# Performance work log

Measured on AMD Instinct MI355X. Metric: run time of the kernel, lower is better.

The kernel has to match this reference:

```python
import jax, jax.numpy as jnp
import numpy as np

B, S, F_IN, F_OUT = 8, 128, 768, 768
NUM_REL = 41           # num_dependencies + 1
NUM_LAYER = 2
N_HEAD, HID = 8, 96    # hidden_dim = embed_dim // n_head
EMB = 768


def setup_inputs() -> dict:
    key = jax.random.key(0)
    ks = jax.random.split(key, 14)
    s = 1.0 / np.sqrt(F_IN)
    inp = {
        "x": jax.random.normal(ks[0], (B, S, F_IN), dtype=jnp.float32),
        "adj": jax.random.uniform(ks[1], (B, NUM_REL, S, S), dtype=jnp.float32),
        "q": jax.random.normal(ks[2], (B, EMB), dtype=jnp.float32),
        # R-GCN params (stacked over layers)
        "w_rgcn": jax.random.uniform(ks[3], (NUM_LAYER, NUM_REL, F_IN, F_OUT), minval=-s, maxval=s),
        "score_w": jax.random.uniform(ks[4], (NUM_LAYER, F_OUT), minval=-s, maxval=s),
        "score_b": jax.random.uniform(ks[5], (NUM_LAYER,), minval=-s, maxval=s),
        # Attention params (stored as [in, out] for x @ W)
        "wk": jax.random.uniform(ks[6], (EMB, N_HEAD * HID), minval=-s, maxval=s),
        "bk": jnp.zeros((N_HEAD * HID,), jnp.float32),
        "wq": jax.random.uniform(ks[7], (EMB, N_HEAD * HID), minval=-s, maxval=s),
        "bq": jnp.zeros((N_HEAD * HID,), jnp.float32),
        "wbil": jax.random.uniform(ks[8], (HID, HID), minval=-1.0 / np.sqrt(HID), maxval=1.0 / np.sqrt(HID)),
        "wproj": jax.random.uniform(ks[9], (N_HEAD * HID, EMB), minval=-s, maxval=s),
        "bproj": jnp.zeros((EMB,), jnp.float32),
    }
    return inp


def _rgcn_layer(h, adj, w, sw, sb):
    # h: [B,S,I]; adj: [B,R,S,S]; w: [R,I,O]
    hidden = jnp.einsum("bsi,rio->brso", h, w)            # per-relation transform
    denom = jnp.sum(adj, axis=3, keepdims=True)           # [B,R,S,1]
    intm = jnp.einsum("brsk,brko->brso", adj, hidden)     # relation-wise aggregation
    div = intm / jnp.where(denom == 0, jnp.ones_like(denom), denom)
    logits = jnp.einsum("brso,o->brs", div, sw) + sb      # score Linear(out->1)
    r_coeffs = jax.nn.softmax(logits, axis=1)             # softmax over relations
    out = jnp.einsum("brso,brs->bso", div, r_coeffs)
    return jax.nn.relu(out)


def _attention(k, q, wk, bk, wq, bq, wbil, wproj, bproj):
    # k: [B,S,E]; q: [B,E] -> [B,1,E]
    q3 = q[:, None, :]
    kx = (k @ wk + bk).reshape(B, S, N_HEAD, HID)
    qx = (q3 @ wq + bq).reshape(B, 1, N_HEAD, HID)
    qw = jnp.einsum("bqhd,de->bqhe", qx, wbil)            # bi_linear score
    score = jnp.einsum("bqhe,bkhe->bhqk", qw, kx)
    attn = jax.nn.softmax(score, axis=-1)
    o = jnp.einsum("bhqk,bkhd->bqhd", attn, kx).reshape(B, 1, N_HEAD * HID)
    return o @ wproj + bproj                              # [B,1,EMB]


def reference(x, adj, q, w_rgcn, score_w, score_b, wk, bk, wq, bq, wbil, wproj, bproj):
    h = x
    for l in range(NUM_LAYER):
        h = _rgcn_layer(h, adj, w_rgcn[l], score_w[l], score_b[l])
    return _attention(h, q, wk, bk, wq, bq, wbil, wproj, bproj)
```

## Files before the change

### kernel.cpp

```cpp
#include <hip/hip_runtime.h>
#include <stdint.h>

#define B_ 8
#define S_ 128
#define R_ 41
#define F_ 768
#define NH_ 8
#define HID_ 96
#define BS_ (B_*S_)
#define SM_SCALE 256.0f
#define NG_ 21

typedef _Float16 f16;
typedef _Float16 f16x8 __attribute__((ext_vector_type(8)));
typedef _Float16 f16x4 __attribute__((ext_vector_type(4)));
typedef float f32x4 __attribute__((ext_vector_type(4)));

#define GLD16(gp, lp) __builtin_amdgcn_global_load_lds((const __attribute__((address_space(1))) uint32_t*)(gp), (__attribute__((address_space(3))) uint32_t*)(lp), 16, 0, 0)

__device__ __forceinline__ float wredsum(float v){
  #pragma unroll
  for (int o=32;o;o>>=1) v += __shfl_down(v,o,64);
  return v;
}

__global__ __launch_bounds__(256) void kConvWV(const float* __restrict__ w, const float* __restrict__ sw,
                                               f16* __restrict__ wT, float* __restrict__ v) {
  int bid = blockIdx.x;
  int it = bid % 12, r = bid / 12;
  __shared__ float t[64*68];
  int tid = threadIdx.x;
  int ri = tid >> 2, c = tid & 3;
  float vacc = 0.f;
  for (int ot = 0; ot < 12; ++ot) {
    const float* src = w + ((size_t)r*F_ + (it*64 + ri))*F_ + ot*64 + c*16;
    const float* swp = sw + ot*64 + c*16;
    __syncthreads();
    #pragma unroll
    for (int j=0;j<4;j++){
      f32x4 v4 = *(const f32x4*)(src + j*4);
      f32x4 s4 = *(const f32x4*)(swp + j*4);
      vacc += v4.x*s4.x + v4.y*s4.y + v4.z*s4.z + v4.w*s4.w;
      *(f32x4*)&t[ri*68 + c*16 + j*4] = v4;
    }
    __syncthreads();
    int ro = tid >> 2;
    f16 outv[16];
    #pragma unroll
    for (int j=0;j<16;j++) outv[j] = (f16)t[(c*16+j)*68 + ro];
    f16* dst = wT + ((size_t)r*F_ + (ot*64+ro))*F_ + it*64 + c*16;
    *(f16x8*)dst = *(f16x8*)&outv[0];
    *(f16x8*)(dst+8) = *(f16x8*)&outv[8];
  }
  vacc += __shfl_down(vacc, 1, 64);
  vacc += __shfl_down(vacc, 2, 64);
  if (c == 0) v[(size_t)r*F_ + it*64 + ri] = vacc;
}

__global__ __launch_bounds__(256) void kConvW(const float* __restrict__ w, f16* __restrict__ wT) {
  int bid = blockIdx.x;
  int ot = bid % 12; int it = (bid/12) % 12; int r = bid / 144;
  __shared__ float t[64*68];
  int tid = threadIdx.x;
  int ri = tid >> 2, c = tid & 3;
  const float* src = w + ((size_t)r*F_ + (it*64 + ri))*F_ + ot*64 + c*16;
  #pragma unroll
  for (int j=0;j<4;j++){
    f32x4 v4 = *(const f32x4*)(src + j*4);
    *(f32x4*)&t[ri*68 + c*16 + j*4] = v4;
  }
  __syncthreads();
  int ro = tid >> 2;
  f16 outv[16];
  #pragma unroll
  for (int j=0;j<16;j++) outv[j] = (f16)t[(c*16+j)*68 + ro];
  f16* dst = wT + ((size_t)r*F_ + (ot*64+ro))*F_ + it*64 + c*16;
  *(f16x8*)dst = *(f16x8*)&outv[0];
  *(f16x8*)(dst+8) = *(f16x8*)&outv[8];
}

template<typename T>
__global__ __launch_bounds__(256) void kTransTo16T(const T* __restrict__ h, f16* __restrict__ hT) {
  int bid = blockIdx.x;
  int st = bid & 1; int ft = (bid>>1) % 12; int b = bid / 24;
  __shared__ f16 t[64*72];
  int tid = threadIdx.x;
  int sl = tid>>2, c = tid&3;
  const T* src = h + ((size_t)b*S_ + st*64 + sl)*F_ + ft*64 + c*16;
  f16 tmp[16];
  #pragma unroll
  for (int j=0;j<16;j++) tmp[j] = (f16)src[j];
  *(f16x8*)&t[sl*72 + c*16]     = *(f16x8*)&tmp[0];
  *(f16x8*)&t[sl*72 + c*16 + 8] = *(f16x8*)&tmp[8];
  __syncthreads();
  int fl = tid>>2;
  f16 outv[16];
  #pragma unroll
  for (int j=0;j<16;j++) outv[j] = t[(c*16+j)*72 + fl];
  f16* dst = hT + ((size_t)b*F_ + ft*64 + fl)*S_ + st*64 + c*16;
  *(f16x8*)dst = *(f16x8*)&outv[0];
  *(f16x8*)(dst+8) = *(f16x8*)&outv[8];
}

__global__ __launch_bounds__(256) void kU(const float* __restrict__ h, const float* __restrict__ v, float* __restrict__ u) {
  int idx = blockIdx.x*4 + (threadIdx.x>>6);
  int lane = threadIdx.x&63;
  int k = idx & 127;
  int br = idx >> 7;
  int r = br % R_;
  int b = br / R_;
  const float* hr = h + ((size_t)b*S_ + k)*F_ + lane*12;
  const float* vr = v + (size_t)r*F_ + lane*12;
  float acc=0.f;
  #pragma unroll
  for (int j=0;j<3;j++){
    f32x4 a = *(const f32x4*)(hr+j*4);
    f32x4 c4 = *(const f32x4*)(vr+j*4);
    acc += a.x*c4.x+a.y*c4.y+a.z*c4.z+a.w*c4.w;
  }
  acc = wredsum(acc);
  if (lane==0) u[idx] = acc;
}

__global__ __launch_bounds__(256) void kLogits(const float* __restrict__ adj, const float* __restrict__ u,
                        const float* __restrict__ sb_all, int l,
                        float* __restrict__ dinv, float* __restrict__ lg) {
  int idx = blockIdx.x*4 + (threadIdx.x>>6);
  int lane = threadIdx.x&63;
  const float* arow = adj + (size_t)idx*S_;
  int br = idx >> 7;
  const float* up = u + (size_t)br*S_;
  float a0 = arow[lane], a1 = arow[lane+64];
  float u0 = up[lane],   u1 = up[lane+64];
  float ssum = a0+a1;
  float sdot = a0*u0 + a1*u1;
  ssum = wredsum(ssum);
  sdot = wredsum(sdot);
  if (lane==0){
    float dv = (ssum==0.0f) ? 1.0f : (1.0f/ssum);
    dinv[idx] = dv;
    lg[idx] = sdot*dv + sb_all[l];
  }
}

__global__ __launch_bounds__(256) void kSoftmaxR(const float* __restrict__ lg, float* __restrict__ c) {
  int t = blockIdx.x*256 + threadIdx.x;
  int b = t >> 7, s = t & 127;
  float vals[R_];
  float mx = -1e30f;
  #pragma unroll
  for (int r=0;r<R_;r++){ float x = lg[((size_t)b*R_+r)*S_ + s]; vals[r]=x; mx = fmaxf(mx,x); }
  float sum=0.f;
  #pragma unroll
  for (int r=0;r<R_;r++){ vals[r] = expf(vals[r]-mx); sum += vals[r]; }
  float inv = 1.0f/sum;
  #pragma unroll
  for (int r=0;r<R_;r++) c[((size_t)b*R_+r)*S_+s] = vals[r]*inv;
}

__global__ __launch_bounds__(256) void kM16(const float* __restrict__ adj, const float* __restrict__ c,
                     const float* __restrict__ dinv, f16* __restrict__ M) {
  int t = blockIdx.x*256 + threadIdx.x;
  int brs = t >> 5; int k4 = (t & 31) * 4;
  float a = SM_SCALE * c[brs] * dinv[brs];
  f32x4 v4 = *(const f32x4*)(adj + (size_t)brs*S_ + k4);
  f16x4 o;
  o[0]=(f16)(v4.x*a); o[1]=(f16)(v4.y*a); o[2]=(f16)(v4.z*a); o[3]=(f16)(v4.w*a);
  *(f16x4*)(M + (size_t)brs*S_ + k4) = o;
}

__global__ __launch_bounds__(256) void kGgemm(const f16* __restrict__ M, const f16* __restrict__ hT, f16* __restrict__ G) {
  __shared__ f16 lds[2*16384];
  f16* lsA = lds;
  f16* lsB = lds + 16384;
  int bid = blockIdx.x;
  int nt = bid % 6; int r = (bid/6) % R_; int b = bid/(6*R_);
  int tid = threadIdx.x, wid = tid>>6, lane = tid&63;
  const f16* Ab = M + (size_t)(b*R_ + r)*(S_*S_);
  const f16* Bb = hT + ((size_t)b*F_ + nt*128)*S_;
  #pragma unroll
  for (int j=0;j<8;j++){
    int qd = wid*8 + j;
    GLD16(Ab + qd*512 + lane*8, lsA + qd*512);
    GLD16(Bb + qd*512 + lane*8, lsB + qd*512);
  }
  __syncthreads();
  f32x4 acc[4][4] = {};
  int wr = wid>>1, wc = wid&1;
  int lr = lane&15, kk0 = (lane>>4)*8;
  #pragma unroll
  for (int ks=0;ks<4;ks++){
    int kk = ks*32 + kk0;
    f16x8 av[4], bv[4];
    #pragma unroll
    for (int i=0;i<4;i++) av[i] = *(const f16x8*)&lsA[(wr*64+i*16+lr)*128 + kk];
    #pragma unroll
    for (int i=0;i<4;i++) bv[i] = *(const f16x8*)&lsB[(wc*64+i*16+lr)*128 + kk];
    #pragma unroll
    for (int mi=0;mi<4;mi++)
      #pragma unroll
      for (int ni=0;ni<4;ni++)
        acc[mi][ni] = __builtin_amdgcn_mfma_f32_16x16x32_f16(av[mi],bv[ni],acc[mi][ni],0,0,0);
  }
  __syncthreads();
  #pragma unroll
  for (int mi=0;mi<4;mi++)
    #pragma unroll
    for (int ni=0;ni<4;ni++){
      int row = wr*64 + mi*16 + (lane>>4)*4;
      int col = wc*64 + ni*16 + lr;
      #pragma unroll
      for (int i=0;i<4;i++)
        lds[(row+i)*136 + col] = (f16)acc[mi][ni][i];
    }
  __syncthreads();
  int row = tid>>1, seg = tid&1;
  f16* dst = G + ((size_t)(b*R_ + r)*S_ + row)*F_ + nt*128 + seg*64;
  const f16* sl = lds + row*136 + seg*64;
  #pragma unroll
  for (int j=0;j<8;j++) *(f16x8*)(dst + j*8) = *(const f16x8*)(sl + j*8);
}

__global__ __launch_bounds__(512,2) void kOutGemm(const f16* __restrict__ G, const f16* __restrict__ WT, float* __restrict__ Cp) {
  __shared__ f16 lsA[256*64];
  __shared__ f16 lsB[256*64];
  int bid = blockIdx.x;
  int t12 = bid % 12, g = bid / 12;
  int nt = t12 % 3, mt = t12 / 3;
  int r0 = (g<20)? 2*g : 40;
  int nr = (g<20)? 2 : 1;
  int tid = threadIdx.x, wid = tid>>6, lane = tid&63;
  size_t abase[4], bbase[4];
  #pragma unroll
  for (int j=0;j<4;j++){
    int chunk = wid*4 + j;
    int arow = mt*256 + chunk*8 + (lane>>3);
    int b = arow >> 7, s = arow & 127;
    abase[j] = ((size_t)b*R_*S_ + s)*(size_t)F_ + (lane&7)*8;
    int orow = nt*256 + chunk*8 + (lane>>3);
    bbase[j] = (size_t)orow*F_ + (lane&7)*8;
  }
  f32x4 acc[8][4] = {};
  int wr = wid>>2, wc = wid&3;
  int lr = lane&15, kk0 = (lane>>4)*8;
  for (int rr=0; rr<nr; ++rr){
    int r = r0 + rr;
    const f16* Ar = G  + (size_t)r*S_*F_;
    const f16* Br = WT + (size_t)r*F_*F_;
    for (int it=0; it<12; ++it){
      #pragma unroll
      for (int j=0;j<4;j++){
        int chunk = wid*4 + j;
        GLD16(Ar + abase[j] + it*64, lsA + chunk*512);
        GLD16(Br + bbase[j] + it*64, lsB + chunk*512);
      }
      __syncthreads();
      #pragma unroll
      for (int ks=0;ks<2;ks++){
        int kk = ks*32 + kk0;
        f16x8 av[8], bv[4];
        #pragma unroll
        for (int i=0;i<8;i++) av[i] = *(const f16x8*)&lsA[(wr*128+i*16+lr)*64 + kk];
        #pragma unroll
        for (int i=0;i<4;i++) bv[i] = *(const f16x8*)&lsB[(wc*64+i*16+lr)*64 + kk];
        #pragma unroll
        for (int mi=0;mi<8;mi++)
          #pragma unroll
          for (int ni=0;ni<4;ni++)
            acc[mi][ni] = __builtin_amdgcn_mfma_f32_16x16x32_f16(av[mi],bv[ni],acc[mi][ni],0,0,0);
      }
      __syncthreads();
    }
  }
  #pragma unroll
  for (int mi=0;mi<8;mi++)
    #pragma unroll
    for (int ni=0;ni<4;ni++){
      int row = mt*256 + wr*128 + mi*16 + (lane>>4)*4;
      int col = nt*256 + wc*64 + ni*16 + lr;
      #pragma unroll
      for (int i=0;i<4;i++)
        Cp[((size_t)g*BS_ + row + i)*F_ + col] = acc[mi][ni][i];
    }
}

__global__ __launch_bounds__(256) void kReduce(const float* __restrict__ Cp, float* __restrict__ h32, f16* __restrict__ h16o) {
  int t = blockIdx.x*256 + threadIdx.x;
  size_t i4 = (size_t)t*4;
  f32x4 s = {};
  #pragma unroll
  for (int g=0; g<NG_; g++){
    f32x4 v4 = *(const f32x4*)(Cp + (size_t)g*BS_*F_ + i4);
    s.x += v4.x; s.y += v4.y; s.z += v4.z; s.w += v4.w;
  }
  const float inv = 1.0f/SM_SCALE;
  f32x4 rr;
  rr.x = fmaxf(s.x*inv, 0.f); rr.y = fmaxf(s.y*inv, 0.f);
  rr.z = fmaxf(s.z*inv, 0.f); rr.w = fmaxf(s.w*inv, 0.f);
  *(f32x4*)(h32 + i4) = rr;
  f16x4 o; o[0]=(f16)rr.x; o[1]=(f16)rr.y; o[2]=(f16)rr.z; o[3]=(f16)rr.w;
  *(f16x4*)(h16o + i4) = o;
}

__global__ __launch_bounds__(256) void kKx(const f16* __restrict__ A, const f16* __restrict__ BT,
                    const float* __restrict__ bias, float* __restrict__ C) {
  __shared__ f16 lsA[128*64];
  __shared__ f16 lsB[128*64];
  int bid = blockIdx.x;
  int nt = bid % 6, mt = bid / 6;
  int tid = threadIdx.x, wid = tid>>6, lane = tid&63;
  size_t abase[4], bbase[4];
  #pragma unroll
  for (int j=0;j<4;j++){
    int qd = wid*4 + j;
    int row = mt*128 + qd*8 + (lane>>3);
    abase[j] = (size_t)row*F_ + (lane&7)*8;
    int o = nt*128 + qd*8 + (lane>>3);
    bbase[j] = (size_t)o*F_ + (lane&7)*8;
  }
  f32x4 acc[4][4] = {};
  int wr = wid>>1, wc = wid&1;
  int lr = lane&15, kk0 = (lane>>4)*8;
  for (int it=0; it<12; ++it){
    #pragma unroll
    for (int j=0;j<4;j++){
      int qd = wid*4+j;
      GLD16(A + abase[j] + it*64, lsA + qd*512);
      GLD16(BT + bbase[j] + it*64, lsB + qd*512);
    }
    __syncthreads();
    #pragma unroll
    for (int ks=0;ks<2;ks++){
      int kk = ks*32 + kk0;
      f16x8 av[4], bv[4];
      #pragma unroll
      for (int i=0;i<4;i++) av[i] = *(const f16x8*)&lsA[(wr*64+i*16+lr)*64 + kk];
      #pragma unroll
      for (int i=0;i<4;i++) bv[i] = *(const f16x8*)&lsB[(wc*64+i*16+lr)*64 + kk];
      #pragma unroll
      for (int mi=0;mi<4;mi++)
        #pragma unroll
        for (int ni=0;ni<4;ni++)
          acc[mi][ni] = __builtin_amdgcn_mfma_f32_16x16x32_f16(av[mi],bv[ni],acc[mi][ni],0,0,0);
    }
    __syncthreads();
  }
  #pragma unroll
  for (int mi=0;mi<4;mi++)
    #pragma unroll
    for (int ni=0;ni<4;ni++){
      int row = mt*128 + wr*64 + mi*16 + (lane>>4)*4;
      int col = nt*128 + wc*64 + ni*16 + lr;
      float bb = bias[col];
      #pragma unroll
      for (int i=0;i<4;i++)
        C[(size_t)(row+i)*F_ + col] = acc[mi][ni][i] + bb;
    }
}

__global__ __launch_bounds__(256) void kAttn(const float* __restrict__ kx, const float* __restrict__ qin,
                      const float* __restrict__ wq, const float* __restrict__ bq,
                      const float* __restrict__ wbil, float* __restrict__ obuf) {
  int bid = blockIdx.x; int h = bid & 7; int b = bid >> 3;
  __shared__ float qx[HID_], qw[HID_], sc[S_];
  __shared__ float smax, ssum;
  int t = threadIdx.x;
  if (t < HID_) {
    float a0=0.f,a1=0.f,a2=0.f,a3=0.f;
    const float* qp = qin + (size_t)b*F_;
    const float* wp = wq + h*HID_ + t;
    for (int i=0;i<F_;i+=4){
      a0 += qp[i]*wp[(size_t)i*F_];
      a1 += qp[i+1]*wp[(size_t)(i+1)*F_];
      a2 += qp[i+2]*wp[(size_t)(i+2)*F_];
      a3 += qp[i+3]*wp[(size_t)(i+3)*F_];
    }
    qx[t] = a0+a1+a2+a3 + bq[h*HID_+t];
  }
  __syncthreads();
  if (t < HID_) {
    float a0=0.f,a1=0.f;
    for (int e=0;e<HID_;e+=2){ a0 += qx[e]*wbil[e*HID_+t]; a1 += qx[e+1]*wbil[(e+1)*HID_+t]; }
    qw[t] = a0+a1;
  }
  __syncthreads();
  if (t < S_) {
    float a0=0.f,a1=0.f;
    const float* kp = kx + ((size_t)b*S_ + t)*F_ + h*HID_;
    for (int e=0;e<HID_;e+=2){ a0 += qw[e]*kp[e]; a1 += qw[e+1]*kp[e+1]; }
    sc[t] = a0+a1;
  }
  __syncthreads();
  if (t < 64) {
    float m = fmaxf(sc[t], sc[t+64]);
    #pragma unroll
    for (int o=32;o;o>>=1) m = fmaxf(m, __shfl_down(m,o,64));
    if (t==0) smax = m;
  }
  __syncthreads();
  if (t < S_) sc[t] = expf(sc[t]-smax);
  __syncthreads();
  if (t < 64) {
    float s = sc[t] + sc[t+64];
    s = wredsum(s);
    if (t==0) ssum = s;
  }
  __syncthreads();
  if (t < HID_) {
    float a0=0.f,a1=0.f;
    const float* kp = kx + ((size_t)b*S_)*F_ + h*HID_ + t;
    for (int k=0;k<S_;k+=2){ a0 += sc[k]*kp[(size_t)k*F_]; a1 += sc[k+1]*kp[(size_t)(k+1)*F_]; }
    obuf[(size_t)b*F_ + h*HID_ + t] = (a0+a1)/ssum;
  }
}

__global__ __launch_bounds__(256) void kProj(const float* __restrict__ obuf, const float* __restrict__ wproj,
                      const float* __restrict__ bproj, float* __restrict__ outp) {
  int bid = blockIdx.x; int b = bid/3, seg = bid%3;
  int t = threadIdx.x;
  __shared__ float ov[F_];
  for (int j=t;j<F_;j+=256) ov[j] = obuf[(size_t)b*F_ + j];
  __syncthreads();
  int col = seg*256 + t;
  float a0=0.f,a1=0.f,a2=0.f,a3=0.f;
  for (int j=0;j<F_;j+=4){
    a0 += ov[j]*wproj[(size_t)j*F_+col];
    a1 += ov[j+1]*wproj[(size_t)(j+1)*F_+col];
    a2 += ov[j+2]*wproj[(size_t)(j+2)*F_+col];
    a3 += ov[j+3]*wproj[(size_t)(j+3)*F_+col];
  }
  outp[(size_t)b*F_ + col] = bproj[col] + a0+a1+a2+a3;
}

extern "C" void kernel_launch(void* const* d_in, const int* in_sizes, int n_in,
                              void* d_out, int out_size, void* d_ws, size_t ws_size,
                              hipStream_t stream) {
  (void)in_sizes; (void)n_in; (void)out_size;
  const float* x      = (const float*)d_in[0];
  const float* adj    = (const float*)d_in[1];
  const float* qin    = (const float*)d_in[2];
  const float* w_rgcn = (const float*)d_in[3];
  const float* score_w= (const float*)d_in[4];
  const float* score_b= (const float*)d_in[5];
  const float* wk     = (const float*)d_in[6];
  const float* bk     = (const float*)d_in[7];
  const float* wq     = (const float*)d_in[8];
  const float* bq     = (const float*)d_in[9];
  const float* wbil   = (const float*)d_in[10];
  const float* wproj  = (const float*)d_in[11];
  const float* bproj  = (const float*)d_in[12];
  float* outp = (float*)d_out;

  char* p = (char*)d_ws;
  auto alloc = [&](size_t bytes)->char* {
    char* r = p; p += (bytes + 255) & ~(size_t)255; return r;
  };
  f16*   w16T  = (f16*)  alloc((size_t)R_*F_*F_*2);
  f16*   G16   = (f16*)  alloc((size_t)B_*R_*S_*F_*2);
  f16*   M16   = (f16*)  alloc((size_t)B_*R_*S_*S_*2);
  float* Cpart = (float*)alloc((size_t)NG_*BS_*F_*4);
  float* h32a  = (float*)alloc((size_t)BS_*F_*4);
  float* h32b  = (float*)alloc((size_t)BS_*F_*4);
  f16*   h16row= (f16*)  alloc((size_t)BS_*F_*2);
  f16*   h16T  = (f16*)  alloc((size_t)BS_*F_*2);
  float* kx    = (float*)alloc((size_t)BS_*F_*4);
  f16*   wkT   = (f16*)  alloc((size_t)F_*F_*2);
  float* vbuf  = (float*)alloc((size_t)R_*F_*4);
  float* ubuf  = (float*)alloc((size_t)B_*R_*S_*4);
  float* dinv  = (float*)alloc((size_t)B_*R_*S_*4);
  float* lgb   = (float*)alloc((size_t)B_*R_*S_*4);
  float* cbuf  = (float*)alloc((size_t)B_*R_*S_*4);
  float* obuf  = (float*)alloc((size_t)B_*F_*4);
  if ((size_t)(p - (char*)d_ws) > ws_size) return;

  const size_t WL = (size_t)R_*F_*F_;

  kConvWV<<<R_*12, 256, 0, stream>>>(w_rgcn, score_w, w16T, vbuf);
  kTransTo16T<float><<<192, 256, 0, stream>>>(x, h16T);
  kU<<<10496, 256, 0, stream>>>(x, vbuf, ubuf);
  kLogits<<<10496, 256, 0, stream>>>(adj, ubuf, score_b, 0, dinv, lgb);
  kSoftmaxR<<<4, 256, 0, stream>>>(lgb, cbuf);
  kM16<<<5248, 256, 0, stream>>>(adj, cbuf, dinv, M16);
  kGgemm<<<B_*R_*6, 256, 0, stream>>>(M16, h16T, G16);
  kOutGemm<<<12*NG_, 512, 0, stream>>>(G16, w16T, Cpart);
  kReduce<<<768, 256, 0, stream>>>(Cpart, h32a, h16row);
  kTransTo16T<f16><<<192, 256, 0, stream>>>(h16row, h16T);

  kConvWV<<<R_*12, 256, 0, stream>>>(w_rgcn + WL, score_w + F_, w16T, vbuf);
  kU<<<10496, 256, 0, stream>>>(h32a, vbuf, ubuf);
  kLogits<<<10496, 256, 0, stream>>>(adj, ubuf, score_b, 1, dinv, lgb);
  kSoftmaxR<<<4, 256, 0, stream>>>(lgb, cbuf);
  kM16<<<5248, 256, 0, stream>>>(adj, cbuf, dinv, M16);
  kGgemm<<<B_*R_*6, 256, 0, stream>>>(M16, h16T, G16);
  kOutGemm<<<12*NG_, 512, 0, stream>>>(G16, w16T, Cpart);
  kReduce<<<768, 256, 0, stream>>>(Cpart, h32b, h16row);

  kConvW<<<144, 256, 0, stream>>>(wk, wkT);
  kKx<<<48, 256, 0, stream>>>(h16row, wkT, bk, kx);
  kAttn<<<64, 256, 0, stream>>>(kx, qin, wq, bq, wbil, obuf);
  kProj<<<24, 256, 0, stream>>>(obuf, wproj, bproj, outp);
}
```

Before: 514.0 us.

## Fuse score/logit/softmax/M kernels and double-buffer LDS in GEMMs

Merges the per-relation score dot product with the adjacency row sums and logits (kUL), and the relation softmax with building the scaled fp16 M matrix (kSM16). This removes two intermediate buffers and several launches per layer. kOutGemm and kKx now use double-buffered LDS so the next K-tile's global-to-LDS loads overlap with the current MFMA work, and kOutGemm raises wave priority around the MFMA section. In exchange, kOutGemm's LDS use doubles to 128KB per block, which may limit occupancy, and the fused kernels launch far fewer blocks, which may reduce parallelism.

```diff
diff --git a/kernel.cpp b/kernel.cpp
--- a/kernel.cpp
+++ b/kernel.cpp
@@ -14,7 +14,9 @@
 typedef _Float16 f16;
 typedef _Float16 f16x8 __attribute__((ext_vector_type(8)));
 typedef _Float16 f16x4 __attribute__((ext_vector_type(4)));
+typedef _Float16 f16x2 __attribute__((ext_vector_type(2)));
 typedef float f32x4 __attribute__((ext_vector_type(4)));
+typedef float f32x2 __attribute__((ext_vector_type(2)));
 
 #define GLD16(gp, lp) __builtin_amdgcn_global_load_lds((const __attribute__((address_space(1))) uint32_t*)(gp), (__attribute__((address_space(3))) uint32_t*)(lp), 16, 0, 0)
 
@@ -102,71 +104,75 @@
   *(f16x8*)(dst+8) = *(f16x8*)&outv[8];
 }
 
-__global__ __launch_bounds__(256) void kU(const float* __restrict__ h, const float* __restrict__ v, float* __restrict__ u) {
-  int idx = blockIdx.x*4 + (threadIdx.x>>6);
-  int lane = threadIdx.x&63;
-  int k = idx & 127;
-  int br = idx >> 7;
-  int r = br % R_;
-  int b = br / R_;
-  const float* hr = h + ((size_t)b*S_ + k)*F_ + lane*12;
-  const float* vr = v + (size_t)r*F_ + lane*12;
-  float acc=0.f;
-  #pragma unroll
-  for (int j=0;j<3;j++){
-    f32x4 a = *(const f32x4*)(hr+j*4);
-    f32x4 c4 = *(const f32x4*)(vr+j*4);
-    acc += a.x*c4.x+a.y*c4.y+a.z*c4.z+a.w*c4.w;
-  }
-  acc = wredsum(acc);
-  if (lane==0) u[idx] = acc;
-}
-
-__global__ __launch_bounds__(256) void kLogits(const float* __restrict__ adj, const float* __restrict__ u,
-                        const float* __restrict__ sb_all, int l,
-                        float* __restrict__ dinv, float* __restrict__ lg) {
-  int idx = blockIdx.x*4 + (threadIdx.x>>6);
-  int lane = threadIdx.x&63;
-  const float* arow = adj + (size_t)idx*S_;
-  int br = idx >> 7;
-  const float* up = u + (size_t)br*S_;
-  float a0 = arow[lane], a1 = arow[lane+64];
-  float u0 = up[lane],   u1 = up[lane+64];
-  float ssum = a0+a1;
-  float sdot = a0*u0 + a1*u1;
-  ssum = wredsum(ssum);
-  sdot = wredsum(sdot);
-  if (lane==0){
-    float dv = (ssum==0.0f) ? 1.0f : (1.0f/ssum);
-    dinv[idx] = dv;
-    lg[idx] = sdot*dv + sb_all[l];
-  }
-}
-
-__global__ __launch_bounds__(256) void kSoftmaxR(const float* __restrict__ lg, float* __restrict__ c) {
-  int t = blockIdx.x*256 + threadIdx.x;
-  int b = t >> 7, s = t & 127;
-  float vals[R_];
-  float mx = -1e30f;
-  #pragma unroll
-  for (int r=0;r<R_;r++){ float x = lg[((size_t)b*R_+r)*S_ + s]; vals[r]=x; mx = fmaxf(mx,x); }
-  float sum=0.f;
-  #pragma unroll
-  for (int r=0;r<R_;r++){ vals[r] = expf(vals[r]-mx); sum += vals[r]; }
-  float inv = 1.0f/sum;
-  #pragma unroll
-  for (int r=0;r<R_;r++) c[((size_t)b*R_+r)*S_+s] = vals[r]*inv;
-}
-
-__global__ __launch_bounds__(256) void kM16(const float* __restrict__ adj, const float* __restrict__ c,
-                     const float* __restrict__ dinv, f16* __restrict__ M) {
-  int t = blockIdx.x*256 + threadIdx.x;
-  int brs = t >> 5; int k4 = (t & 31) * 4;
-  float a = SM_SCALE * c[brs] * dinv[brs];
-  f32x4 v4 = *(const f32x4*)(adj + (size_t)brs*S_ + k4);
-  f16x4 o;
-  o[0]=(f16)(v4.x*a); o[1]=(f16)(v4.y*a); o[2]=(f16)(v4.z*a); o[3]=(f16)(v4.w*a);
-  *(f16x4*)(M + (size_t)brs*S_ + k4) = o;
+__global__ __launch_bounds__(256) void kUL(const float* __restrict__ h, const float* __restrict__ v,
+                    const float* __restrict__ adj, const float* __restrict__ sb_all, int l,
+                    float* __restrict__ dinv, float* __restrict__ lg) {
+  int bid = blockIdx.x;
+  int r = bid % R_, b = bid / R_;
+  __shared__ float v_s[F_];
+  __shared__ float u_s[S_];
+  int tid = threadIdx.x;
+  #pragma unroll
+  for (int j=0;j<3;j++) v_s[tid + j*256] = v[(size_t)r*F_ + tid + j*256];
+  __syncthreads();
+  int wid = tid>>6, lane = tid&63;
+  for (int kl=0; kl<32; ++kl){
+    int k = wid*32 + kl;
+    const float* hr = h + ((size_t)b*S_ + k)*F_ + lane*12;
+    const float* vp = &v_s[lane*12];
+    float acc=0.f;
+    #pragma unroll
+    for (int j=0;j<3;j++){
+      f32x4 a = *(const f32x4*)(hr+j*4);
+      f32x4 c4 = *(const f32x4*)(vp+j*4);
+      acc += a.x*c4.x+a.y*c4.y+a.z*c4.z+a.w*c4.w;
+    }
+    acc = wredsum(acc);
+    if (lane==0) u_s[k] = acc;
+  }
+  __syncthreads();
+  int s = tid>>1, half = tid&1;
+  const float* arow = adj + ((size_t)bid*S_ + s)*S_ + half*64;
+  const float* up = &u_s[half*64];
+  float ssum=0.f, sdot=0.f;
+  #pragma unroll
+  for (int j=0;j<16;j++){
+    f32x4 a = *(const f32x4*)(arow + j*4);
+    ssum += a.x+a.y+a.z+a.w;
+    sdot += a.x*up[j*4] + a.y*up[j*4+1] + a.z*up[j*4+2] + a.w*up[j*4+3];
+  }
+  ssum += __shfl_xor(ssum,1,64);
+  sdot += __shfl_xor(sdot,1,64);
+  if (half==0){
+    float dv = (ssum==0.0f)?1.0f:(1.0f/ssum);
+    dinv[(size_t)bid*S_ + s] = dv;
+    lg[(size_t)bid*S_ + s] = sdot*dv + sb_all[l];
+  }
+}
+
+__global__ __launch_bounds__(64) void kSM16(const float* __restrict__ lg, const float* __restrict__ dinv,
+                     const float* __restrict__ adj, f16* __restrict__ M) {
+  int bid = blockIdx.x;
+  int b = bid >> 7, s = bid & 127;
+  int lane = threadIdx.x;
+  __shared__ float coef[R_];
+  float x = (lane < R_) ? lg[((size_t)b*R_ + lane)*S_ + s] : -1e30f;
+  float m = x;
+  #pragma unroll
+  for (int o=32;o;o>>=1) m = fmaxf(m, __shfl_xor(m,o,64));
+  float e = (lane < R_) ? expf(x - m) : 0.f;
+  float sum = e;
+  #pragma unroll
+  for (int o=32;o;o>>=1) sum += __shfl_xor(sum,o,64);
+  if (lane < R_) coef[lane] = e/sum * SM_SCALE * dinv[((size_t)b*R_ + lane)*S_ + s];
+  __syncthreads();
+  for (int r=0;r<R_;r++){
+    float cc = coef[r];
+    size_t base = (((size_t)(b*R_+r))*S_ + s)*S_ + lane*2;
+    f32x2 a2 = *(const f32x2*)(adj + base);
+    f16x2 o2; o2[0]=(f16)(a2.x*cc); o2[1]=(f16)(a2.y*cc);
+    *(f16x2*)(M + base) = o2;
+  }
 }
 
 __global__ __launch_bounds__(256) void kGgemm(const f16* __restrict__ M, const f16* __restrict__ hT, f16* __restrict__ G) {
@@ -222,8 +228,7 @@
 }
 
 __global__ __launch_bounds__(512,2) void kOutGemm(const f16* __restrict__ G, const f16* __restrict__ WT, float* __restrict__ Cp) {
-  __shared__ f16 lsA[256*64];
-  __shared__ f16 lsB[256*64];
+  __shared__ f16 ls[2][2][256*64];
   int bid = blockIdx.x;
   int t12 = bid % 12, g = bid / 12;
   int nt = t12 % 3, mt = t12 / 3;
@@ -243,34 +248,41 @@
   f32x4 acc[8][4] = {};
   int wr = wid>>2, wc = wid&3;
   int lr = lane&15, kk0 = (lane>>4)*8;
-  for (int rr=0; rr<nr; ++rr){
-    int r = r0 + rr;
+  int nsteps = nr*12;
+  auto STAGE = [&](int bf, int step){
+    int r = r0 + step/12, it = step%12;
     const f16* Ar = G  + (size_t)r*S_*F_;
     const f16* Br = WT + (size_t)r*F_*F_;
-    for (int it=0; it<12; ++it){
-      #pragma unroll
-      for (int j=0;j<4;j++){
-        int chunk = wid*4 + j;
-        GLD16(Ar + abase[j] + it*64, lsA + chunk*512);
-        GLD16(Br + bbase[j] + it*64, lsB + chunk*512);
-      }
-      __syncthreads();
-      #pragma unroll
-      for (int ks=0;ks<2;ks++){
-        int kk = ks*32 + kk0;
-        f16x8 av[8], bv[4];
+    #pragma unroll
+    for (int j=0;j<4;j++){
+      int chunk = wid*4 + j;
+      GLD16(Ar + abase[j] + it*64, &ls[bf][0][chunk*512]);
+      GLD16(Br + bbase[j] + it*64, &ls[bf][1][chunk*512]);
+    }
+  };
+  STAGE(0, 0);
+  __syncthreads();
+  int cur = 0;
+  for (int step=0; step<nsteps; ++step){
+    if (step+1 < nsteps) STAGE(cur^1, step+1);
+    __builtin_amdgcn_s_setprio(1);
+    #pragma unroll
+    for (int ks=0;ks<2;ks++){
+      int kk = ks*32 + kk0;
+      f16x8 av[8], bv[4];
+      #pragma unroll
+      for (int i=0;i<8;i++) av[i] = *(const f16x8*)&ls[cur][0][(wr*128+i*16+lr)*64 + kk];
+      #pragma unroll
+      for (int i=0;i<4;i++) bv[i] = *(const f16x8*)&ls[cur][1][(wc*64+i*16+lr)*64 + kk];
+      #pragma unroll
+      for (int mi=0;mi<8;mi++)
         #pragma unroll
-        for (int i=0;i<8;i++) av[i] = *(const f16x8*)&lsA[(wr*128+i*16+lr)*64 + kk];
-        #pragma unroll
-        for (int i=0;i<4;i++) bv[i] = *(const f16x8*)&lsB[(wc*64+i*16+lr)*64 + kk];
-        #pragma unroll
-        for (int mi=0;mi<8;mi++)
-          #pragma unroll
-          for (int ni=0;ni<4;ni++)
-            acc[mi][ni] = __builtin_amdgcn_mfma_f32_16x16x32_f16(av[mi],bv[ni],acc[mi][ni],0,0,0);
-      }
-      __syncthreads();
-    }
+        for (int ni=0;ni<4;ni++)
+          acc[mi][ni] = __builtin_amdgcn_mfma_f32_16x16x32_f16(av[mi],bv[ni],acc[mi][ni],0,0,0);
+    }
+    __builtin_amdgcn_s_setprio(0);
+    __syncthreads();
+    cur ^= 1;
   }
   #pragma unroll
   for (int mi=0;mi<8;mi++)
@@ -304,8 +316,7 @@
 
 __global__ __launch_bounds__(256) void kKx(const f16* __restrict__ A, const f16* __restrict__ BT,
                     const float* __restrict__ bias, float* __restrict__ C) {
-  __shared__ f16 lsA[128*64];
-  __shared__ f16 lsB[128*64];
+  __shared__ f16 ls[2][2][128*64];
   int bid = blockIdx.x;
   int nt = bid % 6, mt = bid / 6;
   int tid = threadIdx.x, wid = tid>>6, lane = tid&63;
@@ -321,22 +332,27 @@
   f32x4 acc[4][4] = {};
   int wr = wid>>1, wc = wid&1;
   int lr = lane&15, kk0 = (lane>>4)*8;
-  for (int it=0; it<12; ++it){
+  auto STAGE = [&](int bf, int it){
     #pragma unroll
     for (int j=0;j<4;j++){
       int qd = wid*4+j;
-      GLD16(A + abase[j] + it*64, lsA + qd*512);
-      GLD16(BT + bbase[j] + it*64, lsB + qd*512);
-    }
-    __syncthreads();
+      GLD16(A + abase[j] + it*64, &ls[bf][0][qd*512]);
+      GLD16(BT + bbase[j] + it*64, &ls[bf][1][qd*512]);
+    }
+  };
+  STAGE(0, 0);
+  __syncthreads();
+  int cur = 0;
+  for (int it=0; it<12; ++it){
+    if (it+1 < 12) STAGE(cur^1, it+1);
     #pragma unroll
     for (int ks=0;ks<2;ks++){
       int kk = ks*32 + kk0;
       f16x8 av[4], bv[4];
       #pragma unroll
-      for (int i=0;i<4;i++) av[i] = *(const f16x8*)&lsA[(wr*64+i*16+lr)*64 + kk];
-      #pragma unroll
-      for (int i=0;i<4;i++) bv[i] = *(const f16x8*)&lsB[(wc*64+i*16+lr)*64 + kk];
+      for (int i=0;i<4;i++) av[i] = *(const f16x8*)&ls[cur][0][(wr*64+i*16+lr)*64 + kk];
+      #pragma unroll
+      for (int i=0;i<4;i++) bv[i] = *(const f16x8*)&ls[cur][1][(wc*64+i*16+lr)*64 + kk];
       #pragma unroll
       for (int mi=0;mi<4;mi++)
         #pragma unroll
@@ -344,6 +360,7 @@
           acc[mi][ni] = __builtin_amdgcn_mfma_f32_16x16x32_f16(av[mi],bv[ni],acc[mi][ni],0,0,0);
     }
     __syncthreads();
+    cur ^= 1;
   }
   #pragma unroll
   for (int mi=0;mi<4;mi++)
@@ -466,10 +483,8 @@
   float* kx    = (float*)alloc((size_t)BS_*F_*4);
   f16*   wkT   = (f16*)  alloc((size_t)F_*F_*2);
   float* vbuf  = (float*)alloc((size_t)R_*F_*4);
-  float* ubuf  = (float*)alloc((size_t)B_*R_*S_*4);
   float* dinv  = (float*)alloc((size_t)B_*R_*S_*4);
   float* lgb   = (float*)alloc((size_t)B_*R_*S_*4);
-  float* cbuf  = (float*)alloc((size_t)B_*R_*S_*4);
   float* obuf  = (float*)alloc((size_t)B_*F_*4);
   if ((size_t)(p - (char*)d_ws) > ws_size) return;
 
@@ -477,20 +492,16 @@
 
   kConvWV<<<R_*12, 256, 0, stream>>>(w_rgcn, score_w, w16T, vbuf);
   kTransTo16T<float><<<192, 256, 0, stream>>>(x, h16T);
-  kU<<<10496, 256, 0, stream>>>(x, vbuf, ubuf);
-  kLogits<<<10496, 256, 0, stream>>>(adj, ubuf, score_b, 0, dinv, lgb);
-  kSoftmaxR<<<4, 256, 0, stream>>>(lgb, cbuf);
-  kM16<<<5248, 256, 0, stream>>>(adj, cbuf, dinv, M16);
+  kUL<<<B_*R_, 256, 0, stream>>>(x, vbuf, adj, score_b, 0, dinv, lgb);
+  kSM16<<<B_*S_, 64, 0, stream>>>(lgb, dinv, adj, M16);
   kGgemm<<<B_*R_*6, 256, 0, stream>>>(M16, h16T, G16);
   kOutGemm<<<12*NG_, 512, 0, stream>>>(G16, w16T, Cpart);
   kReduce<<<768, 256, 0, stream>>>(Cpart, h32a, h16row);
   kTransTo16T<f16><<<192, 256, 0, stream>>>(h16row, h16T);
 
   kConvWV<<<R_*12, 256, 0, stream>>>(w_rgcn + WL, score_w + F_, w16T, vbuf);
-  kU<<<10496, 256, 0, stream>>>(h32a, vbuf, ubuf);
-  kLogits<<<10496, 256, 0, stream>>>(adj, ubuf, score_b, 1, dinv, lgb);
-  kSoftmaxR<<<4, 256, 0, stream>>>(lgb, cbuf);
-  kM16<<<5248, 256, 0, stream>>>(adj, cbuf, dinv, M16);
+  kUL<<<B_*R_, 256, 0, stream>>>(h32a, vbuf, adj, score_b, 1, dinv, lgb);
+  kSM16<<<B_*S_, 64, 0, stream>>>(lgb, dinv, adj, M16);
   kGgemm<<<B_*R_*6, 256, 0, stream>>>(M16, h16T, G16);
   kOutGemm<<<12*NG_, 512, 0, stream>>>(G16, w16T, Cpart);
   kReduce<<<768, 256, 0, stream>>>(Cpart, h32b, h16row);
```

Result: faster. 483.6 us (-5.9%).
